# Kernel tuning notes

Hardware: AMD Instinct MI355X
Metric: run time of the kernel (lower is better)

## Reference

```python
import jax, jax.numpy as jnp
import numpy as np

EPS = 1e-12  # matches torch F.normalize clamp_min eps


def setup_inputs() -> dict:
    key = jax.random.key(0)
    k1, k2 = jax.random.split(key)
    T, H, E = 32768, 4096, 128
    x = jax.random.normal(k1, (T, H), dtype=jnp.float32)
    W = jax.random.normal(k2, (E, H), dtype=jnp.float32) * 0.02  # router_linear.weight [E, H]
    router_bias = jnp.zeros((E,), dtype=jnp.float32)
    return {"x": x, "W": W, "router_bias": router_bias, "k": 8}


def reference(x, W, router_bias, k):
    # logits = x @ W^T : [T, E]
    logits = jnp.einsum('th,eh->te', x, W)
    scores = jax.nn.sigmoid(logits)
    balancing_scores = scores + router_bias  # bias only steers selection
    _, topk_idx = jax.lax.top_k(balancing_scores, k)          # [T, k]
    final_w = jnp.take_along_axis(scores, topk_idx, axis=-1)   # gather raw scores
    denom = jnp.maximum(jnp.sum(jnp.abs(final_w), axis=-1, keepdims=True), EPS)
    final_w = final_w / denom  # L1 normalize (F.normalize p=1)
    return final_w, topk_idx
```

## Files before the change

kernel.cpp:

```cpp
#include <hip/hip_runtime.h>
#include <math.h>

#define TOPK 8
#define NE   128
#define MARGIN 1e-5f

typedef _Float16 h8 __attribute__((ext_vector_type(8)));
typedef _Float16 h4 __attribute__((ext_vector_type(4)));
typedef float    f4 __attribute__((ext_vector_type(4)));

__device__ __forceinline__ int swz(int row, int kb) {
  return row * 128 + (kb ^ ((row & 7) << 4));
}

#define GLOAD_LDS16(g, l)                                              \
  __builtin_amdgcn_global_load_lds(                                    \
      (const __attribute__((address_space(1))) void*)(g),              \
      (__attribute__((address_space(3))) void*)(l), 16, 0, 0)

__global__ __launch_bounds__(256) void router_wsplit(
    const float* __restrict__ W, _Float16* __restrict__ whi,
    _Float16* __restrict__ wlo, int n4) {
  const int i = blockIdx.x * 256 + threadIdx.x;
  if (i < n4) {
    const float4 v = ((const float4*)W)[i];
    h4 hi, lo;
#pragma unroll
    for (int q = 0; q < 4; ++q) {
      const float vq = ((const float*)&v)[q];
      const _Float16 h = (_Float16)vq;
      hi[q] = h;
      lo[q] = (_Float16)((vq - (float)h) * 2048.0f);
    }
    ((h4*)whi)[i] = hi;
    ((h4*)wlo)[i] = lo;
  }
}

__global__ __launch_bounds__(512, 2) void router_pass1(
    const float* __restrict__ x,
    const _Float16* __restrict__ whi,
    const _Float16* __restrict__ wlo,
    const float* __restrict__ bias,
    float* __restrict__ out_w, float* __restrict__ out_i,
    unsigned int* __restrict__ mask, int T, int H) {
  __shared__ char lds[81920];

  const int tid = threadIdx.x;
  const int t0  = blockIdx.x * 64;
  const int l   = tid & 63;
  const int wv  = tid >> 6;
  const int wm  = wv & 1;
  const int wn  = wv >> 1;

  const int xrow = tid >> 3;
  const float* xptr = x + (size_t)(t0 + xrow) * H + (tid & 7) * 8;
  const int aw = swz(xrow, (tid & 7) * 16);

  int soff0, soff1;
  {
    const int o0  = (wv * 2) * 1024 + l * 16;
    const int r0  = o0 >> 7;
    soff0 = r0 * (H * 2) + ((o0 & 127) ^ ((r0 & 7) << 4));
    const int o1  = (wv * 2 + 1) * 1024 + l * 16;
    const int r1  = o1 >> 7;
    soff1 = r1 * (H * 2) + ((o1 & 127) ^ ((r1 & 7) << 4));
  }
  const int dst0 = (wv * 2) * 1024;
  const int dst1 = (wv * 2 + 1) * 1024;

  f4 acc1[2][2], acc2[2][2];
#pragma unroll
  for (int mt = 0; mt < 2; ++mt)
#pragma unroll
    for (int nt = 0; nt < 2; ++nt) { acc1[mt][nt] = (f4)0.0f; acc2[mt][nt] = (f4)0.0f; }

  GLOAD_LDS16((const char*)whi + soff0, lds + 16384 + dst0);
  GLOAD_LDS16((const char*)whi + soff1, lds + 16384 + dst1);
  GLOAD_LDS16((const char*)wlo + soff0, lds + 32768 + dst0);
  GLOAD_LDS16((const char*)wlo + soff1, lds + 32768 + dst1);
  float4 pxA0 = *(const float4*)(xptr);
  float4 pxA1 = *(const float4*)(xptr + 4);
  float4 pxB0 = *(const float4*)(xptr + 64);
  float4 pxB1 = *(const float4*)(xptr + 68);

#define ITER(K0, PX0, PX1, CUR)                                               \
  {                                                                           \
          \
    if ((K0) + 64 < H)                                                        \
      asm volatile("s_waitcnt vmcnt(2) lgkmcnt(0)" ::: "memory");             \
    else                                                                      \
      asm volatile("s_waitcnt vmcnt(0) lgkmcnt(0)" ::: "memory");             \
    __builtin_amdgcn_s_barrier();                                             \
    __builtin_amdgcn_sched_barrier(0);                                        \
               \
    if ((K0) + 64 < H) {                                                      \
      const char* whb = (const char*)whi + (size_t)((K0) + 64) * 2;           \
      const char* wlb = (const char*)wlo + (size_t)((K0) + 64) * 2;           \
      const int nb = 16384 + ((CUR) ^ 1) * 32768;                             \
      GLOAD_LDS16(whb + soff0, lds + nb + dst0);                              \
      GLOAD_LDS16(whb + soff1, lds + nb + dst1);                              \
      GLOAD_LDS16(wlb + soff0, lds + nb + 16384 + dst0);                      \
      GLOAD_LDS16(wlb + soff1, lds + nb + 16384 + dst1);                      \
    }                                                                         \
    {                     \
      h8 hi, lo;                                                              \
      const float* pv0 = (const float*)&PX0;                                  \
      const float* pv1 = (const float*)&PX1;                                  \
      _Pragma("unroll")                                                       \
      for (int q = 0; q < 4; ++q) {                                           \
        const _Float16 h0 = (_Float16)pv0[q];                                 \
        const _Float16 h1 = (_Float16)pv1[q];                                 \
        hi[q] = h0; hi[4 + q] = h1;                                           \
        lo[q]     = (_Float16)((pv0[q] - (float)h0) * 2048.0f);               \
        lo[4 + q] = (_Float16)((pv1[q] - (float)h1) * 2048.0f);               \
      }                                                                       \
      *(h8*)(lds + aw)        = hi;                                           \
      *(h8*)(lds + 8192 + aw) = lo;                                           \
    }                                                                         \
                                        \
    if ((K0) + 128 < H) {                                                     \
      PX0 = *(const float4*)(xptr + (K0) + 128);                              \
      PX1 = *(const float4*)(xptr + (K0) + 132);                              \
    }                                                                         \
         \
    asm volatile("s_waitcnt lgkmcnt(0)" ::: "memory");                        \
    __builtin_amdgcn_s_barrier();                                             \
    __builtin_amdgcn_sched_barrier(0);                                        \
    {                                               \
      const int bhi = 16384 + (CUR) * 32768;                                  \
      _Pragma("unroll")                                                       \
      for (int ks = 0; ks < 2; ++ks) {                                        \
        const int kb = ks * 64 + ((l >> 4) * 16);                             \
        h8 Ah[2], Al[2];                                                      \
        _Pragma("unroll")                                                     \
        for (int mt = 0; mt < 2; ++mt) {                                      \
          const int row = wm * 32 + mt * 16 + (l & 15);                       \
          Ah[mt] = *(const h8*)(lds +        swz(row, kb));                   \
          Al[mt] = *(const h8*)(lds + 8192 + swz(row, kb));                   \
        }                                                                     \
        _Pragma("unroll")                                                     \
        for (int nt = 0; nt < 2; ++nt) {                                      \
          const int er = wn * 32 + nt * 16 + (l & 15);                        \
          const h8 Bh = *(const h8*)(lds + bhi         + swz(er, kb));        \
          const h8 Bl = *(const h8*)(lds + bhi + 16384 + swz(er, kb));        \
          _Pragma("unroll")                                                   \
          for (int mt = 0; mt < 2; ++mt) {                                    \
            acc1[mt][nt] = __builtin_amdgcn_mfma_f32_16x16x32_f16(Ah[mt], Bh, acc1[mt][nt], 0, 0, 0); \
            acc2[mt][nt] = __builtin_amdgcn_mfma_f32_16x16x32_f16(Ah[mt], Bl, acc2[mt][nt], 0, 0, 0); \
            acc2[mt][nt] = __builtin_amdgcn_mfma_f32_16x16x32_f16(Al[mt], Bh, acc2[mt][nt], 0, 0, 0); \
          }                                                                   \
        }                                                                     \
      }                                                                       \
    }                                                                         \
  }

  for (int k0 = 0; k0 < H; k0 += 128) {
    ITER(k0,      pxA0, pxA1, 0)
    ITER(k0 + 64, pxB0, pxB1, 1)
  }
#undef ITER

  __syncthreads();
  float* logits = (float*)lds;
  unsigned char* flg = (unsigned char*)(lds + 33792);
#pragma unroll
  for (int mt = 0; mt < 2; ++mt)
#pragma unroll
    for (int nt = 0; nt < 2; ++nt)
#pragma unroll
      for (int r = 0; r < 4; ++r) {
        const int row = wm * 32 + mt * 16 + (l >> 4) * 4 + r;
        const int col = wn * 32 + nt * 16 + (l & 15);
        logits[row * 132 + col] = acc1[mt][nt][r] + acc2[mt][nt][r] * (1.0f / 2048.0f);
      }
  __syncthreads();

  const int tx    = tid & 15;
  const int g     = tid >> 4;
  const int lane  = tid & 63;
  const int gbase = lane & 48;

  float biasr[8];
#pragma unroll
  for (int j = 0; j < 4; ++j) {
    biasr[j]     = bias[tx * 4 + j];
    biasr[4 + j] = bias[64 + tx * 4 + j];
  }

#pragma unroll
  for (int it = 0; it < 2; ++it) {
    const int tok = g * 2 + it;
    const float4 lo4 = *(const float4*)(logits + tok * 132 + tx * 4);
    const float4 hi4 = *(const float4*)(logits + tok * 132 + 64 + tx * 4);
    float sc[8], bal[8];
#pragma unroll
    for (int j = 0; j < 4; ++j) {
      sc[j]     = 1.f / (1.f + expf(-((const float*)&lo4)[j]));
      sc[4 + j] = 1.f / (1.f + expf(-((const float*)&hi4)[j]));
    }
#pragma unroll
    for (int j = 0; j < 8; ++j) bal[j] = sc[j] + biasr[j];

    float myw[TOPK];
    int   myid[TOPK];
    float prev = 0.f;
    int   flagged = 0;
#pragma unroll
    for (int r = 0; r < TOPK + 1; ++r) {
      float bv = bal[0];
      int   bi = tx * 4;
#pragma unroll
      for (int j = 1; j < 8; ++j) {
        const int ej = (j < 4) ? (tx * 4 + j) : (64 + tx * 4 + (j - 4));
        if (bal[j] > bv) { bv = bal[j]; bi = ej; }
      }
#pragma unroll
      for (int m = 1; m <= 8; m <<= 1) {
        const float ov = __shfl_xor(bv, m);
        const int   oi = __shfl_xor(bi, m);
        if (ov > bv || (ov == bv && oi < bi)) { bv = ov; bi = oi; }
      }
      if (r > 0 && (prev - bv) < MARGIN) flagged = 1;
      prev = bv;
      if (r < TOPK) {
        const int ls = (bi < 64) ? (bi >> 2) : ((bi - 64) >> 2);
        const int jt = (bi < 64) ? (bi & 3) : (4 + ((bi - 64) & 3));
        const float a0s = (jt & 1) ? sc[1] : sc[0];
        const float a1s = (jt & 1) ? sc[3] : sc[2];
        const float a2s = (jt & 1) ? sc[5] : sc[4];
        const float a3s = (jt & 1) ? sc[7] : sc[6];
        const float b0s = (jt & 2) ? a1s : a0s;
        const float b1s = (jt & 2) ? a3s : a2s;
        const float sv = (jt & 4) ? b1s : b0s;
        const float sw = __shfl(sv, gbase | ls);
        myw[r]  = sw;
        myid[r] = bi;
#pragma unroll
        for (int j = 0; j < 8; ++j)
          if (tx == ls && j == jt) bal[j] = -INFINITY;
      }
    }

    if (tx == 0) {
      float den = 0.f;
#pragma unroll
      for (int r = 0; r < TOPK; ++r) den += fabsf(myw[r]);
      den = fmaxf(den, 1e-12f);
      const int t = t0 + tok;
      float4* wo = (float4*)(out_w + (size_t)t * TOPK);
      float4* io = (float4*)(out_i + (size_t)t * TOPK);
      wo[0] = make_float4(myw[0] / den, myw[1] / den, myw[2] / den, myw[3] / den);
      wo[1] = make_float4(myw[4] / den, myw[5] / den, myw[6] / den, myw[7] / den);
      io[0] = make_float4((float)myid[0], (float)myid[1], (float)myid[2], (float)myid[3]);
      io[1] = make_float4((float)myid[4], (float)myid[5], (float)myid[6], (float)myid[7]);
      flg[tok] = (unsigned char)flagged;
    }
  }

  __syncthreads();
  if (tid < 2) {
    unsigned int wbits = 0;
#pragma unroll
    for (int b = 0; b < 32; ++b)
      wbits |= (flg[tid * 32 + b] ? 1u : 0u) << b;
    mask[blockIdx.x * 2 + tid] = wbits;
  }
}

__global__ __launch_bounds__(1024) void router_compact(
    const unsigned int* __restrict__ mask, int* __restrict__ cnt,
    int* __restrict__ flags, int nwords) {
  __shared__ int wsum[17];
  const int tid = threadIdx.x;
  unsigned int w = (tid < nwords) ? mask[tid] : 0u;
  const int c = __popc(w);
  const int lane = tid & 63;
  const int wv   = tid >> 6;
  int inc = c;
#pragma unroll
  for (int m = 1; m < 64; m <<= 1) {
    const int v = __shfl_up(inc, m);
    if (lane >= m) inc += v;
  }
  if (lane == 63) wsum[wv + 1] = inc;
  __syncthreads();
  if (tid == 0) {
    wsum[0] = 0;
    for (int i = 1; i <= 16; ++i) wsum[i] += wsum[i - 1];
    cnt[0] = wsum[16];
  }
  __syncthreads();
  int off = wsum[wv] + inc - c;
  while (w) {
    const int b = __ffs(w) - 1;
    w &= w - 1u;
    flags[off++] = tid * 32 + b;
  }
}

__global__ __launch_bounds__(256) void router_pass2(
    const float* __restrict__ x, const float* __restrict__ W,
    const float* __restrict__ bias,
    float* __restrict__ out_w, float* __restrict__ out_i,
    const int* __restrict__ cnt, const int* __restrict__ flags, int H) {
  __shared__ float  xs[4096];
  __shared__ double red[NE];

  const int tid = threadIdx.x;
  const int e   = tid & 127;
  const int h   = tid >> 7;
  const int count = cnt[0];

  for (int i = blockIdx.x; i < count; i += gridDim.x) {
    const int t = flags[i];

    __syncthreads();
    {
      const float* xp = x + (size_t)t * H;
#pragma unroll
      for (int c = 0; c < 4; ++c) {
        const int fi = (c * 256 + tid) * 4;
        *(float4*)(xs + fi) = *(const float4*)(xp + fi);
      }
    }
    __syncthreads();

    double a0 = 0.0, a1 = 0.0, a2 = 0.0, a3 = 0.0;
    {
      const float* wp = W + (size_t)e * H + h * 2048;
      const float* xb = xs + h * 2048;
      for (int kk = 0; kk < 2048; kk += 4) {
        const float4 wv = *(const float4*)(wp + kk);
        const float4 xv = *(const float4*)(xb + kk);
        a0 = fma((double)xv.x, (double)wv.x, a0);
        a1 = fma((double)xv.y, (double)wv.y, a1);
        a2 = fma((double)xv.z, (double)wv.z, a2);
        a3 = fma((double)xv.w, (double)wv.w, a3);
      }
    }
    const double a = (a0 + a1) + (a2 + a3);

    if (h == 1) red[e] = a;
    __syncthreads();
    if (h == 0) red[e] = 1.0 / (1.0 + exp(-(a + red[e])));
    __syncthreads();

    if (tid < 64) {
      const int l = tid;
      const double s0 = red[l];
      const double s1 = red[64 + l];
      double g0 = s0 + (double)bias[l];
      double g1 = s1 + (double)bias[64 + l];
      double myw[TOPK]; int myid[TOPK];
#pragma unroll
      for (int r = 0; r < TOPK; ++r) {
        double bv; int bi;
        if (g1 > g0) { bv = g1; bi = 64 + l; } else { bv = g0; bi = l; }
#pragma unroll
        for (int m = 1; m <= 32; m <<= 1) {
          const double ov = __shfl_xor(bv, m);
          const int    oi = __shfl_xor(bi, m);
          if (ov > bv || (ov == bv && oi < bi)) { bv = ov; bi = oi; }
        }
        const int ls   = bi & 63;
        const int slot = bi >> 6;
        const double sv = slot ? s1 : s0;
        const double sw = __shfl(sv, ls);
        myw[r]  = sw;
        myid[r] = bi;
        if (l == ls) { if (slot) g1 = -INFINITY; else g0 = -INFINITY; }
      }
      if (l == 0) {
        double den = 0.0;
#pragma unroll
        for (int r = 0; r < TOPK; ++r) den += fabs(myw[r]);
        den = fmax(den, 1e-12);
#pragma unroll
        for (int r = 0; r < TOPK; ++r) {
          out_w[(size_t)t * TOPK + r] = (float)(myw[r] / den);
          out_i[(size_t)t * TOPK + r] = (float)myid[r];
        }
      }
    }
  }
}

extern "C" void kernel_launch(void* const* d_in, const int* in_sizes, int n_in,
                              void* d_out, int out_size, void* d_ws, size_t ws_size,
                              hipStream_t stream) {
  const float* x    = (const float*)d_in[0];
  const float* W    = (const float*)d_in[1];
  const float* bias = (const float*)d_in[2];
  const int E = in_sizes[2];
  const int H = in_sizes[1] / E;
  const int T = in_sizes[0] / H;
  (void)E; (void)n_in; (void)ws_size; (void)out_size;

  float* out_w = (float*)d_out;
  float* out_i = out_w + (size_t)T * TOPK;

  char* ws = (char*)d_ws;
  _Float16* whi = (_Float16*)ws;
  _Float16* wlo = (_Float16*)(ws + (1 << 20));
  unsigned int* mask = (unsigned int*)(ws + (2 << 20));
  const int nwords = (T + 31) / 32;
  int* cnt   = (int*)(ws + (2 << 20) + nwords * 4);
  int* flags = (int*)(ws + (2 << 20) + nwords * 4 + 16);

  const int n4 = (E * H) / 4;
  router_wsplit<<<dim3((n4 + 255) / 256), dim3(256), 0, stream>>>(W, whi, wlo, n4);
  router_pass1<<<dim3(T / 64), dim3(512), 0, stream>>>(x, whi, wlo, bias, out_w, out_i, mask, T, H);
  router_compact<<<dim3(1), dim3(1024), 0, stream>>>(mask, cnt, flags, nwords);
  router_pass2<<<dim3(2048), dim3(256), 0, stream>>>(x, W, bias, out_w, out_i, cnt, flags, H);
}
```

Before: 240.1 us.

## Drop compaction kernel; batch four flagged tokens per pass2 block, raise MFMA priority

Removes the single-block compaction launch. Pass2 now reads the flag bitmask directly, with one block per 16 tokens that exits early when none of its tokens are flagged. Each block processes up to four flagged tokens at once, so every W load is reused across four token dot products in fp64. It also raises wave priority around the MFMA section of pass1. The cost is a launch of many mostly-empty blocks and more LDS per block, which may reduce occupancy.

```diff
diff --git a/kernel.cpp b/kernel.cpp
--- a/kernel.cpp
+++ b/kernel.cpp
@@ -127,8 +127,9 @@
     asm volatile("s_waitcnt lgkmcnt(0)" ::: "memory");                        \
     __builtin_amdgcn_s_barrier();                                             \
     __builtin_amdgcn_sched_barrier(0);                                        \
-    {                                               \
+    {                        \
       const int bhi = 16384 + (CUR) * 32768;                                  \
+      __builtin_amdgcn_s_setprio(1);                                          \
       _Pragma("unroll")                                                       \
       for (int ks = 0; ks < 2; ++ks) {                                        \
         const int kb = ks * 64 + ((l >> 4) * 16);                             \
@@ -152,6 +153,7 @@
           }                                                                   \
         }                                                                     \
       }                                                                       \
+      __builtin_amdgcn_s_setprio(0);                                          \
     }                                                                         \
   }
 
@@ -268,118 +270,114 @@
   }
 }
 
-__global__ __launch_bounds__(1024) void router_compact(
-    const unsigned int* __restrict__ mask, int* __restrict__ cnt,
-    int* __restrict__ flags, int nwords) {
-  __shared__ int wsum[17];
-  const int tid = threadIdx.x;
-  unsigned int w = (tid < nwords) ? mask[tid] : 0u;
-  const int c = __popc(w);
-  const int lane = tid & 63;
-  const int wv   = tid >> 6;
-  int inc = c;
-#pragma unroll
-  for (int m = 1; m < 64; m <<= 1) {
-    const int v = __shfl_up(inc, m);
-    if (lane >= m) inc += v;
-  }
-  if (lane == 63) wsum[wv + 1] = inc;
-  __syncthreads();
-  if (tid == 0) {
-    wsum[0] = 0;
-    for (int i = 1; i <= 16; ++i) wsum[i] += wsum[i - 1];
-    cnt[0] = wsum[16];
-  }
-  __syncthreads();
-  int off = wsum[wv] + inc - c;
-  while (w) {
-    const int b = __ffs(w) - 1;
-    w &= w - 1u;
-    flags[off++] = tid * 32 + b;
-  }
-}
-
 __global__ __launch_bounds__(256) void router_pass2(
     const float* __restrict__ x, const float* __restrict__ W,
     const float* __restrict__ bias,
     float* __restrict__ out_w, float* __restrict__ out_i,
-    const int* __restrict__ cnt, const int* __restrict__ flags, int H) {
-  __shared__ float  xs[4096];
-  __shared__ double red[NE];
+    const unsigned int* __restrict__ mask, int H) {
+  __shared__ float  xs[4 * 4096];
+  __shared__ double red[4 * NE];
 
   const int tid = threadIdx.x;
   const int e   = tid & 127;
   const int h   = tid >> 7;
-  const int count = cnt[0];
-
-  for (int i = blockIdx.x; i < count; i += gridDim.x) {
-    const int t = flags[i];
+
+  unsigned int bits =
+      (mask[blockIdx.x >> 1] >> ((blockIdx.x & 1) * 16)) & 0xFFFFu;
+  if (bits == 0u) return;
+  const int base = blockIdx.x * 16;
+
+  while (bits) {
+    int tk0, tk1, tk2, tk3;
+    {
+      int b = __ffs(bits) - 1; bits &= bits - 1u; tk0 = base + b;
+      b = __ffs(bits); tk1 = b ? base + b - 1 : tk0; if (b) bits &= bits - 1u;
+      b = __ffs(bits); tk2 = b ? base + b - 1 : tk0; if (b) bits &= bits - 1u;
+      b = __ffs(bits); tk3 = b ? base + b - 1 : tk0; if (b) bits &= bits - 1u;
+    }
+    int toks[4] = {tk0, tk1, tk2, tk3};
 
     __syncthreads();
-    {
-      const float* xp = x + (size_t)t * H;
+#pragma unroll
+    for (int t = 0; t < 4; ++t) {
+      const float* xp = x + (size_t)toks[t] * H;
 #pragma unroll
       for (int c = 0; c < 4; ++c) {
         const int fi = (c * 256 + tid) * 4;
-        *(float4*)(xs + fi) = *(const float4*)(xp + fi);
+        *(float4*)(xs + t * 4096 + fi) = *(const float4*)(xp + fi);
       }
     }
     __syncthreads();
 
-    double a0 = 0.0, a1 = 0.0, a2 = 0.0, a3 = 0.0;
+    double a[4] = {0.0, 0.0, 0.0, 0.0};
     {
       const float* wp = W + (size_t)e * H + h * 2048;
       const float* xb = xs + h * 2048;
       for (int kk = 0; kk < 2048; kk += 4) {
         const float4 wv = *(const float4*)(wp + kk);
-        const float4 xv = *(const float4*)(xb + kk);
-        a0 = fma((double)xv.x, (double)wv.x, a0);
-        a1 = fma((double)xv.y, (double)wv.y, a1);
-        a2 = fma((double)xv.z, (double)wv.z, a2);
-        a3 = fma((double)xv.w, (double)wv.w, a3);
-      }
-    }
-    const double a = (a0 + a1) + (a2 + a3);
-
-    if (h == 1) red[e] = a;
+#pragma unroll
+        for (int t = 0; t < 4; ++t) {
+          const float4 xv = *(const float4*)(xb + t * 4096 + kk);
+          a[t] = fma((double)xv.x, (double)wv.x, a[t]);
+          a[t] = fma((double)xv.y, (double)wv.y, a[t]);
+          a[t] = fma((double)xv.z, (double)wv.z, a[t]);
+          a[t] = fma((double)xv.w, (double)wv.w, a[t]);
+        }
+      }
+    }
+
+    if (h == 1) {
+#pragma unroll
+      for (int t = 0; t < 4; ++t) red[t * NE + e] = a[t];
+    }
     __syncthreads();
-    if (h == 0) red[e] = 1.0 / (1.0 + exp(-(a + red[e])));
+    if (h == 0) {
+#pragma unroll
+      for (int t = 0; t < 4; ++t)
+        red[t * NE + e] = 1.0 / (1.0 + exp(-(a[t] + red[t * NE + e])));
+    }
     __syncthreads();
 
     if (tid < 64) {
       const int l = tid;
-      const double s0 = red[l];
-      const double s1 = red[64 + l];
-      double g0 = s0 + (double)bias[l];
-      double g1 = s1 + (double)bias[64 + l];
-      double myw[TOPK]; int myid[TOPK];
-#pragma unroll
-      for (int r = 0; r < TOPK; ++r) {
-        double bv; int bi;
-        if (g1 > g0) { bv = g1; bi = 64 + l; } else { bv = g0; bi = l; }
-#pragma unroll
-        for (int m = 1; m <= 32; m <<= 1) {
-          const double ov = __shfl_xor(bv, m);
-          const int    oi = __shfl_xor(bi, m);
-          if (ov > bv || (ov == bv && oi < bi)) { bv = ov; bi = oi; }
+      const double b0d = (double)bias[l];
+      const double b1d = (double)bias[64 + l];
+#pragma unroll
+      for (int t = 0; t < 4; ++t) {
+        const double s0 = red[t * NE + l];
+        const double s1 = red[t * NE + 64 + l];
+        double g0 = s0 + b0d;
+        double g1 = s1 + b1d;
+        double myw[TOPK]; int myid[TOPK];
+#pragma unroll
+        for (int r = 0; r < TOPK; ++r) {
+          double bv; int bi;
+          if (g1 > g0) { bv = g1; bi = 64 + l; } else { bv = g0; bi = l; }
+#pragma unroll
+          for (int m = 1; m <= 32; m <<= 1) {
+            const double ov = __shfl_xor(bv, m);
+            const int    oi = __shfl_xor(bi, m);
+            if (ov > bv || (ov == bv && oi < bi)) { bv = ov; bi = oi; }
+          }
+          const int ls   = bi & 63;
+          const int slot = bi >> 6;
+          const double sv = slot ? s1 : s0;
+          const double sw = __shfl(sv, ls);
+          myw[r]  = sw;
+          myid[r] = bi;
+          if (l == ls) { if (slot) g1 = -INFINITY; else g0 = -INFINITY; }
         }
-        const int ls   = bi & 63;
-        const int slot = bi >> 6;
-        const double sv = slot ? s1 : s0;
-        const double sw = __shfl(sv, ls);
-        myw[r]  = sw;
-        myid[r] = bi;
-        if (l == ls) { if (slot) g1 = -INFINITY; else g0 = -INFINITY; }
-      }
-      if (l == 0) {
-        double den = 0.0;
-#pragma unroll
-        for (int r = 0; r < TOPK; ++r) den += fabs(myw[r]);
-        den = fmax(den, 1e-12);
-#pragma unroll
-        for (int r = 0; r < TOPK; ++r) {
-          out_w[(size_t)t * TOPK + r] = (float)(myw[r] / den);
-          out_i[(size_t)t * TOPK + r] = (float)myid[r];
+        if (l == 0) {
+          double den = 0.0;
+#pragma unroll
+          for (int r = 0; r < TOPK; ++r) den += fabs(myw[r]);
+          den = fmax(den, 1e-12);
+          const int tok = toks[t];
+#pragma unroll
+          for (int r = 0; r < TOPK; ++r) {
+            out_w[(size_t)tok * TOPK + r] = (float)(myw[r] / den);
+            out_i[(size_t)tok * TOPK + r] = (float)myid[r];
+          }
         }
       }
     }
@@ -404,13 +402,9 @@
   _Float16* whi = (_Float16*)ws;
   _Float16* wlo = (_Float16*)(ws + (1 << 20));
   unsigned int* mask = (unsigned int*)(ws + (2 << 20));
-  const int nwords = (T + 31) / 32;
-  int* cnt   = (int*)(ws + (2 << 20) + nwords * 4);
-  int* flags = (int*)(ws + (2 << 20) + nwords * 4 + 16);
 
   const int n4 = (E * H) / 4;
   router_wsplit<<<dim3((n4 + 255) / 256), dim3(256), 0, stream>>>(W, whi, wlo, n4);
   router_pass1<<<dim3(T / 64), dim3(512), 0, stream>>>(x, whi, wlo, bias, out_w, out_i, mask, T, H);
-  router_compact<<<dim3(1), dim3(1024), 0, stream>>>(mask, cnt, flags, nwords);
-  router_pass2<<<dim3(2048), dim3(256), 0, stream>>>(x, W, bias, out_w, out_i, cnt, flags, H);
+  router_pass2<<<dim3(T / 16), dim3(256), 0, stream>>>(x, W, bias, out_w, out_i, mask, H);
 }
```

After: 296.1 us. 1.23x slower.

## Halve K-tile to 32, double-buffer A tile, drop second barrier for higher occupancy

Applied to the files above, without the earlier changes.

The GEMM main loop now uses a K-step of 32 instead of 64. The fp16-split x tile is double-buffered alongside W, which removes the second barrier per iteration. LDS drops from 80KB to 48KB with a new two-rows-per-line swizzle, and launch bounds are raised to aim for more resident blocks per CU to hide memory latency. In exchange it runs twice as many barriers and iterations, issues smaller loads per step, and the higher occupancy target may cause register spills.

```diff
diff --git a/kernel.cpp b/kernel.cpp
--- a/kernel.cpp
+++ b/kernel.cpp
@@ -9,8 +9,9 @@
 typedef _Float16 h4 __attribute__((ext_vector_type(4)));
 typedef float    f4 __attribute__((ext_vector_type(4)));
 
-__device__ __forceinline__ int swz(int row, int kb) {
-  return row * 128 + (kb ^ ((row & 7) << 4));
+__device__ __forceinline__ int adr(int row, int kb) {
+  const int line = row >> 1;
+  return line * 128 + ((((row & 1) << 6) | kb) ^ ((line & 7) << 4));
 }
 
 #define GLOAD_LDS16(g, l)                                              \
@@ -37,14 +38,14 @@
   }
 }
 
-__global__ __launch_bounds__(512, 2) void router_pass1(
+__global__ __launch_bounds__(512, 6) void router_pass1(
     const float* __restrict__ x,
     const _Float16* __restrict__ whi,
     const _Float16* __restrict__ wlo,
     const float* __restrict__ bias,
     float* __restrict__ out_w, float* __restrict__ out_i,
     unsigned int* __restrict__ mask, int T, int H) {
-  __shared__ char lds[81920];
+  __shared__ char lds[49152];
 
   const int tid = threadIdx.x;
   const int t0  = blockIdx.x * 64;
@@ -53,21 +54,17 @@
   const int wm  = wv & 1;
   const int wn  = wv >> 1;
 
-  const int xrow = tid >> 3;
-  const float* xptr = x + (size_t)(t0 + xrow) * H + (tid & 7) * 8;
-  const int aw = swz(xrow, (tid & 7) * 16);
-
-  int soff0, soff1;
+  const float* xptr = x + (size_t)(t0 + (tid >> 3)) * H + (tid & 7) * 4;
+  const int awA = adr(tid >> 3, (tid & 7) * 8);
+
+  int soff;
   {
-    const int o0  = (wv * 2) * 1024 + l * 16;
-    const int r0  = o0 >> 7;
-    soff0 = r0 * (H * 2) + ((o0 & 127) ^ ((r0 & 7) << 4));
-    const int o1  = (wv * 2 + 1) * 1024 + l * 16;
-    const int r1  = o1 >> 7;
-    soff1 = r1 * (H * 2) + ((o1 & 127) ^ ((r1 & 7) << 4));
-  }
-  const int dst0 = (wv * 2) * 1024;
-  const int dst1 = (wv * 2 + 1) * 1024;
+    const int o    = tid * 16;
+    const int line = o >> 7;
+    const int un   = (o & 127) ^ ((line & 7) << 4);
+    soff = (line * 2 + (un >> 6)) * (H * 2) + (un & 63);
+  }
+  const int wvbase = wv * 1024;
 
   f4 acc1[2][2], acc2[2][2];
 #pragma unroll
@@ -75,89 +72,84 @@
 #pragma unroll
     for (int nt = 0; nt < 2; ++nt) { acc1[mt][nt] = (f4)0.0f; acc2[mt][nt] = (f4)0.0f; }
 
-  GLOAD_LDS16((const char*)whi + soff0, lds + 16384 + dst0);
-  GLOAD_LDS16((const char*)whi + soff1, lds + 16384 + dst1);
-  GLOAD_LDS16((const char*)wlo + soff0, lds + 32768 + dst0);
-  GLOAD_LDS16((const char*)wlo + soff1, lds + 32768 + dst1);
-  float4 pxA0 = *(const float4*)(xptr);
-  float4 pxA1 = *(const float4*)(xptr + 4);
-  float4 pxB0 = *(const float4*)(xptr + 64);
-  float4 pxB1 = *(const float4*)(xptr + 68);
-
-#define ITER(K0, PX0, PX1, CUR)                                               \
+  GLOAD_LDS16((const char*)whi + soff, lds + 16384 + wvbase);
+  GLOAD_LDS16((const char*)wlo + soff, lds + 24576 + wvbase);
+  float4 px = *(const float4*)(xptr);
+  {
+    const float* pv = (const float*)&px;
+    h4 hi4, lo4;
+#pragma unroll
+    for (int q = 0; q < 4; ++q) {
+      const _Float16 hh = (_Float16)pv[q];
+      hi4[q] = hh;
+      lo4[q] = (_Float16)((pv[q] - (float)hh) * 2048.0f);
+    }
+    *(h4*)(lds + awA)        = hi4;
+    *(h4*)(lds + 4096 + awA) = lo4;
+  }
+  px = *(const float4*)(xptr + 32);
+
+#define ITER(K0, CUR)                                                         \
   {                                                                           \
-          \
-    if ((K0) + 64 < H)                                                        \
-      asm volatile("s_waitcnt vmcnt(2) lgkmcnt(0)" ::: "memory");             \
+    \
+    if ((K0) + 32 < H)                                                        \
+      asm volatile("s_waitcnt vmcnt(1) lgkmcnt(0)" ::: "memory");             \
     else                                                                      \
       asm volatile("s_waitcnt vmcnt(0) lgkmcnt(0)" ::: "memory");             \
     __builtin_amdgcn_s_barrier();                                             \
     __builtin_amdgcn_sched_barrier(0);                                        \
-               \
-    if ((K0) + 64 < H) {                                                      \
-      const char* whb = (const char*)whi + (size_t)((K0) + 64) * 2;           \
-      const char* wlb = (const char*)wlo + (size_t)((K0) + 64) * 2;           \
-      const int nb = 16384 + ((CUR) ^ 1) * 32768;                             \
-      GLOAD_LDS16(whb + soff0, lds + nb + dst0);                              \
-      GLOAD_LDS16(whb + soff1, lds + nb + dst1);                              \
-      GLOAD_LDS16(wlb + soff0, lds + nb + 16384 + dst0);                      \
-      GLOAD_LDS16(wlb + soff1, lds + nb + 16384 + dst1);                      \
-    }                                                                         \
-    {                     \
-      h8 hi, lo;                                                              \
-      const float* pv0 = (const float*)&PX0;                                  \
-      const float* pv1 = (const float*)&PX1;                                  \
+    if ((K0) + 32 < H) {                                                      \
+                 \
+      const char* whb = (const char*)whi + (size_t)((K0) + 32) * 2;           \
+      const char* wlb = (const char*)wlo + (size_t)((K0) + 32) * 2;           \
+      const int nb = 16384 + ((CUR) ^ 1) * 16384;                             \
+      GLOAD_LDS16(whb + soff, lds + nb + wvbase);                             \
+      GLOAD_LDS16(wlb + soff, lds + nb + 8192 + wvbase);                      \
+                                     \
+      const float* pv = (const float*)&px;                                    \
+      h4 hi4, lo4;                                                            \
       _Pragma("unroll")                                                       \
       for (int q = 0; q < 4; ++q) {                                           \
-        const _Float16 h0 = (_Float16)pv0[q];                                 \
-        const _Float16 h1 = (_Float16)pv1[q];                                 \
-        hi[q] = h0; hi[4 + q] = h1;                                           \
-        lo[q]     = (_Float16)((pv0[q] - (float)h0) * 2048.0f);               \
-        lo[4 + q] = (_Float16)((pv1[q] - (float)h1) * 2048.0f);               \
+        const _Float16 hh = (_Float16)pv[q];                                  \
+        hi4[q] = hh;                                                          \
+        lo4[q] = (_Float16)((pv[q] - (float)hh) * 2048.0f);                   \
       }                                                                       \
-      *(h8*)(lds + aw)        = hi;                                           \
-      *(h8*)(lds + 8192 + aw) = lo;                                           \
+      const int ab = ((CUR) ^ 1) * 8192;                                      \
+      *(h4*)(lds + ab + awA)        = hi4;                                    \
+      *(h4*)(lds + ab + 4096 + awA) = lo4;                                    \
     }                                                                         \
-                                        \
-    if ((K0) + 128 < H) {                                                     \
-      PX0 = *(const float4*)(xptr + (K0) + 128);                              \
-      PX1 = *(const float4*)(xptr + (K0) + 132);                              \
-    }                                                                         \
-         \
-    asm volatile("s_waitcnt lgkmcnt(0)" ::: "memory");                        \
-    __builtin_amdgcn_s_barrier();                                             \
-    __builtin_amdgcn_sched_barrier(0);                                        \
-    {                                               \
-      const int bhi = 16384 + (CUR) * 32768;                                  \
+                                                 \
+    if ((K0) + 64 < H) px = *(const float4*)(xptr + (K0) + 64);               \
+                                           \
+    {                                                                         \
+      const int abase = (CUR) * 8192;                                         \
+      const int bbase = 16384 + (CUR) * 16384;                                \
+      const int kbb = (l >> 4) * 16;                                          \
+      h8 Ah[2], Al[2];                                                        \
       _Pragma("unroll")                                                       \
-      for (int ks = 0; ks < 2; ++ks) {                                        \
-        const int kb = ks * 64 + ((l >> 4) * 16);                             \
-        h8 Ah[2], Al[2];                                                      \
+      for (int mt = 0; mt < 2; ++mt) {                                        \
+        const int row = wm * 32 + mt * 16 + (l & 15);                         \
+        Ah[mt] = *(const h8*)(lds + abase +        adr(row, kbb));            \
+        Al[mt] = *(const h8*)(lds + abase + 4096 + adr(row, kbb));            \
+      }                                                                       \
+      _Pragma("unroll")                                                       \
+      for (int nt = 0; nt < 2; ++nt) {                                        \
+        const int er = wn * 32 + nt * 16 + (l & 15);                          \
+        const h8 Bh = *(const h8*)(lds + bbase +        adr(er, kbb));        \
+        const h8 Bl = *(const h8*)(lds + bbase + 8192 + adr(er, kbb));        \
         _Pragma("unroll")                                                     \
         for (int mt = 0; mt < 2; ++mt) {                                      \
-          const int row = wm * 32 + mt * 16 + (l & 15);                       \
-          Ah[mt] = *(const h8*)(lds +        swz(row, kb));                   \
-          Al[mt] = *(const h8*)(lds + 8192 + swz(row, kb));                   \
-        }                                                                     \
-        _Pragma("unroll")                                                     \
-        for (int nt = 0; nt < 2; ++nt) {                                      \
-          const int er = wn * 32 + nt * 16 + (l & 15);                        \
-          const h8 Bh = *(const h8*)(lds + bhi         + swz(er, kb));        \
-          const h8 Bl = *(const h8*)(lds + bhi + 16384 + swz(er, kb));        \
-          _Pragma("unroll")                                                   \
-          for (int mt = 0; mt < 2; ++mt) {                                    \
-            acc1[mt][nt] = __builtin_amdgcn_mfma_f32_16x16x32_f16(Ah[mt], Bh, acc1[mt][nt], 0, 0, 0); \
-            acc2[mt][nt] = __builtin_amdgcn_mfma_f32_16x16x32_f16(Ah[mt], Bl, acc2[mt][nt], 0, 0, 0); \
-            acc2[mt][nt] = __builtin_amdgcn_mfma_f32_16x16x32_f16(Al[mt], Bh, acc2[mt][nt], 0, 0, 0); \
-          }                                                                   \
+          acc1[mt][nt] = __builtin_amdgcn_mfma_f32_16x16x32_f16(Ah[mt], Bh, acc1[mt][nt], 0, 0, 0); \
+          acc2[mt][nt] = __builtin_amdgcn_mfma_f32_16x16x32_f16(Ah[mt], Bl, acc2[mt][nt], 0, 0, 0); \
+          acc2[mt][nt] = __builtin_amdgcn_mfma_f32_16x16x32_f16(Al[mt], Bh, acc2[mt][nt], 0, 0, 0); \
         }                                                                     \
       }                                                                       \
     }                                                                         \
   }
 
-  for (int k0 = 0; k0 < H; k0 += 128) {
-    ITER(k0,      pxA0, pxA1, 0)
-    ITER(k0 + 64, pxB0, pxB1, 1)
+  for (int k0 = 0; k0 < H; k0 += 64) {
+    ITER(k0,      0)
+    ITER(k0 + 32, 1)
   }
 #undef ITER
 
```

Result: slower. 269.2 us (+12.2%).
